# Kernel optimization log

Hardware: AMD Instinct MI355X
Metric: run time of the kernel (lower is better)

## Reference

```python
import jax, jax.numpy as jnp
import numpy as np

B, CIN, COUT, H, W = 64, 96, 96, 56, 56
MID = 192            # in_channels * expansion
SE_GROUPS = 12       # _nearest_divisor(192, 12)
SE_RED = 24          # ceil(max(192//8,4)/12)*12
EPS = 1e-5


def _apply_bn(x, p):
    # p: [4, C] = (gamma, beta, running_mean, running_var); eval-mode BN
    scale = p[0] * jax.lax.rsqrt(p[3] + EPS)
    shift = p[1] - p[2] * scale
    return x * scale[None, :, None, None] + shift[None, :, None, None]


def _shift_groups(x):
    h, w = x.shape[2], x.shape[3]
    x0, x1, x2, x3 = jnp.split(x, 4, axis=1)
    up = jnp.pad(x0, ((0, 0), (0, 0), (1, 0), (0, 0)))[:, :, :h, :]
    left = jnp.pad(x1, ((0, 0), (0, 0), (0, 0), (1, 0)))[:, :, :, :w]
    down = jnp.pad(x2, ((0, 0), (0, 0), (0, 1), (0, 0)))[:, :, 1:, :]
    right = jnp.pad(x3, ((0, 0), (0, 0), (0, 0), (0, 1)))[:, :, :, 1:]
    return jnp.concatenate([up, left, down, right], axis=1)


def _channel_shuffle(x, groups=4):
    b, c, h, w = x.shape
    x = x.reshape(b, groups, c // groups, h, w)
    x = jnp.transpose(x, (0, 2, 1, 3, 4))
    return x.reshape(b, c, h, w)


def _grouped_1x1(v, w, b, groups):
    # v: [B, Cin]; w: [Cout, Cin//groups, 1, 1]
    bsz = v.shape[0]
    cout = w.shape[0]
    vg = v.reshape(bsz, groups, -1)
    wg = w[:, :, 0, 0].reshape(groups, cout // groups, -1)
    out = jnp.einsum('bgi,goi->bgo', vg, wg).reshape(bsz, cout)
    return out + b


def _forward(x, expand_w, expand_bn, dw_w, dw_bn, id_w, id_bn, merge_bn,
             se_red_w, se_red_b, se_exp_w, se_exp_b, proj_w, proj_bn):
    # 1x1 expansion + BN + SiLU
    out = jnp.einsum('bchw,oc->bohw', x, expand_w[:, :, 0, 0])
    out = jax.nn.silu(_apply_bn(out, expand_bn))
    # shift-mix + channel shuffle (zero-FLOP data movement)
    out = _channel_shuffle(_shift_groups(out), groups=4)
    # depthwise 3x3 branch + BN
    dw = jax.lax.conv_general_dilated(
        out, dw_w, window_strides=(1, 1), padding=((1, 1), (1, 1)),
        feature_group_count=MID, dimension_numbers=('NCHW', 'OIHW', 'NCHW'))
    dw = _apply_bn(dw, dw_bn)
    # identity depthwise 1x1 branch (per-channel scale) + BN
    idb = _apply_bn(out * id_w[:, 0, 0, 0][None, :, None, None], id_bn)
    out = jax.nn.silu(_apply_bn(dw + idb, merge_bn))
    # grouped SE gating
    se = jnp.mean(out, axis=(2, 3))                     # [B, MID]
    se = jax.nn.relu(_grouped_1x1(se, se_red_w, se_red_b, SE_GROUPS))
    se = jax.nn.sigmoid(_grouped_1x1(se, se_exp_w, se_exp_b, SE_GROUPS))
    out = out * se[:, :, None, None]
    # 1x1 project + BN + residual + activation
    out = jnp.einsum('bchw,oc->bohw', out, proj_w[:, :, 0, 0])
    out = _apply_bn(out, proj_bn)
    out = out + x  # use_residual: stride==1 and in==out
    return jax.nn.silu(out)


def setup_inputs() -> dict:
    key = jax.random.key(0)
    ks = jax.random.split(key, 16)

    def bn_params(k, c):
        k1, k2, k3, k4 = jax.random.split(k, 4)
        gamma = 1.0 + 0.1 * jax.random.normal(k1, (c,), jnp.float32)
        beta = 0.1 * jax.random.normal(k2, (c,), jnp.float32)
        mean = 0.1 * jax.random.normal(k3, (c,), jnp.float32)
        var = 0.5 + jax.random.uniform(k4, (c,), jnp.float32)
        return jnp.stack([gamma, beta, mean, var])

    return {
        'x': jax.random.normal(ks[0], (B, CIN, H, W), jnp.float32),
        'expand_w': 0.1 * jax.random.normal(ks[1], (MID, CIN, 1, 1), jnp.float32),
        'expand_bn': bn_params(ks[2], MID),
        'dw_w': 0.2 * jax.random.normal(ks[3], (MID, 1, 3, 3), jnp.float32),
        'dw_bn': bn_params(ks[4], MID),
        'id_w': 0.2 * jax.random.normal(ks[5], (MID, 1, 1, 1), jnp.float32),
        'id_bn': bn_params(ks[6], MID),
        'merge_bn': bn_params(ks[7], MID),
        'se_red_w': 0.2 * jax.random.normal(ks[8], (SE_RED, MID // SE_GROUPS, 1, 1), jnp.float32),
        'se_red_b': 0.05 * jax.random.normal(ks[9], (SE_RED,), jnp.float32),
        'se_exp_w': 0.2 * jax.random.normal(ks[10], (MID, SE_RED // SE_GROUPS, 1, 1), jnp.float32),
        'se_exp_b': 0.05 * jax.random.normal(ks[11], (MID,), jnp.float32),
        'proj_w': 0.1 * jax.random.normal(ks[12], (COUT, MID, 1, 1), jnp.float32),
        'proj_bn': bn_params(ks[13], COUT),
    }


def reference(x, expand_w, expand_bn, dw_w, dw_bn, id_w, id_bn, merge_bn,
              se_red_w, se_red_b, se_exp_w, se_exp_b, proj_w, proj_bn):
    return _forward(x, expand_w, expand_bn, dw_w, dw_bn, id_w, id_bn, merge_bn,
                    se_red_w, se_red_b, se_exp_w, se_exp_b, proj_w, proj_bn)
```

## Files before the change

### kernel.cpp

```cpp
#include <hip/hip_runtime.h>
#include <hip/hip_bf16.h>

#define BB   64
#define CING 96
#define MIDC 192
#define HH   56
#define WWD  56
#define HWSZ (HH*WWD)
#define COUTC 96
#define BNEPS 1e-5f

typedef __attribute__((ext_vector_type(8))) short short8;
typedef __attribute__((ext_vector_type(8))) unsigned short ushort8v;
typedef __attribute__((ext_vector_type(4))) float float4v;
typedef unsigned short ushort_t;
typedef unsigned int uint_t;
typedef __attribute__((ext_vector_type(4))) uint_t uint4v;

__device__ __forceinline__ float siluf(float v){
    return v * __builtin_amdgcn_rcpf(1.f + __expf(-v));
}
__device__ __forceinline__ ushort_t f2bs(float f){
    uint_t u = __float_as_uint(f);
    uint_t r = u + 0x7FFFu + ((u >> 16) & 1u);
    return (ushort_t)(r >> 16);
}
__device__ __forceinline__ float bs2f(ushort_t u){
    return __uint_as_float(((uint_t)u) << 16);
}
__device__ __forceinline__ uint_t pkbf(float a, float b){
    __hip_bfloat162 h = __float22bfloat162_rn(make_float2(a, b));
    union { __hip_bfloat162 h; uint_t u; } cv; cv.h = h; return cv.u;
}
__device__ __forceinline__ float bslo(uint_t x){ return __uint_as_float(x << 16); }
__device__ __forceinline__ float bshi(uint_t x){ return __uint_as_float(x & 0xFFFF0000u); }

__global__ __launch_bounds__(256) void k0_setup(
    const float* __restrict__ expand_w, const float* __restrict__ expand_bn,
    const float* __restrict__ dw_w, const float* __restrict__ dw_bn,
    const float* __restrict__ id_w, const float* __restrict__ id_bn,
    const float* __restrict__ merge_bn,
    const float* __restrict__ proj_w, const float* __restrict__ proj_bn,
    ushort_t* __restrict__ Aexp, float* __restrict__ ebias,
    float* __restrict__ w9f, float* __restrict__ cstf,
    ushort_t* __restrict__ Aproj, float* __restrict__ pscf, float* __restrict__ pshf)
{
    int i = blockIdx.x*256 + threadIdx.x;
    if (i < 4608) {
        int m = i/24, kq = (i%24)*4;
        int ic = (m&3)*48 + (m>>2);
        float sc0 = expand_bn[ic]*rsqrtf(expand_bn[3*MIDC+ic]+BNEPS);
        #pragma unroll
        for (int j=0;j<4;j++) Aexp[m*96+kq+j] = f2bs(expand_w[ic*96+kq+j]*sc0);
        if (kq==0) ebias[m] = expand_bn[MIDC+ic] - expand_bn[2*MIDC+ic]*sc0;
    } else if (i < 9216) {
        int ii = i-4608; int m = ii/48, kq = (ii%48)*4;
        #pragma unroll
        for (int j=0;j<4;j++) Aproj[m*MIDC+kq+j] = f2bs(proj_w[m*MIDC+kq+j]);
        if (kq==0){
            float sc = proj_bn[m]*rsqrtf(proj_bn[3*COUTC+m]+BNEPS);
            pscf[m]=sc; pshf[m]=proj_bn[COUTC+m]-proj_bn[2*COUTC+m]*sc;
        }
    } else if (i < 9408) {
        int oc = i-9216;
        float sc1 = dw_bn[oc]    * rsqrtf(dw_bn[3*MIDC+oc]    + BNEPS);
        float sh1 = dw_bn[MIDC+oc]    - dw_bn[2*MIDC+oc]*sc1;
        float sc2 = id_bn[oc]    * rsqrtf(id_bn[3*MIDC+oc]    + BNEPS);
        float sh2 = id_bn[MIDC+oc]    - id_bn[2*MIDC+oc]*sc2;
        float sc3 = merge_bn[oc] * rsqrtf(merge_bn[3*MIDC+oc] + BNEPS);
        float sh3 = merge_bn[MIDC+oc] - merge_bn[2*MIDC+oc]*sc3;
        float A = sc3*sc1;
        #pragma unroll
        for (int j=0;j<9;j++) w9f[oc*9+j] = A*dw_w[oc*9+j];
        w9f[oc*9+4] += sc3*sc2*id_w[oc];
        cstf[oc] = sc3*(sh1+sh2) + sh3;
    }
}

#define LDB1T 104
__global__ __launch_bounds__(256, 2) void k1_expand(
    const float* __restrict__ x,
    const ushort_t* __restrict__ Aexp,
    const float* __restrict__ ebias,
    ushort_t* __restrict__ EY)
{
    __shared__ __align__(16) ushort_t BsT[64*LDB1T];
    __shared__ float ebL[MIDC];
    const int t = threadIdx.x;
    const int p0 = blockIdx.x*64, b = blockIdx.y;

    if (t < MIDC) ebL[t] = ebias[t];
    {
        const int pq = t & 15;
        const int cb = (t >> 4) * 6;
        const float* xp0 = x + ((size_t)(b*CING + cb))*HWSZ + p0 + pq*4;
        float4v xv[6];
        #pragma unroll
        for (int j = 0; j < 6; j++)
            xv[j] = *(const float4v*)(xp0 + (size_t)j*HWSZ);
        #pragma unroll
        for (int px = 0; px < 4; px++) {
            const int n = pq*4 + px;
            uint_t w0 = pkbf(xv[0][px], xv[1][px]);
            uint_t w1 = pkbf(xv[2][px], xv[3][px]);
            uint_t w2 = pkbf(xv[4][px], xv[5][px]);
            uint_t* dst = (uint_t*)(&BsT[n*LDB1T + cb]);
            dst[0] = w0; dst[1] = w1; dst[2] = w2;
        }
    }

    const int lane = t & 63, wv = t >> 6;
    const int l = lane & 15, q = lane >> 4;
    short8 afc[3], afn[3];
    #pragma unroll
    for (int mi = 0; mi < 3; mi++)
        afc[mi] = *(const short8*)(Aexp + ((wv*3+mi)*16 + l)*96 + q*8);
    __syncthreads();

    float4v acc[3][4];
    #pragma unroll
    for (int mi=0;mi<3;mi++)
        #pragma unroll
        for (int nt=0;nt<4;nt++) acc[mi][nt] = (float4v){0.f,0.f,0.f,0.f};
    #pragma unroll
    for (int ks = 0; ks < 3; ks++) {
        if (ks < 2) {
            #pragma unroll
            for (int mi = 0; mi < 3; mi++)
                afn[mi] = *(const short8*)(Aexp + ((wv*3+mi)*16 + l)*96 + (ks+1)*32 + q*8);
        }
        const int k0 = ks*32;
        short8 bf[4];
        #pragma unroll
        for (int nt = 0; nt < 4; nt++)
            bf[nt] = *(const short8*)(&BsT[(nt*16 + l)*LDB1T + k0 + q*8]);
        #pragma unroll
        for (int mi = 0; mi < 3; mi++)
            #pragma unroll
            for (int nt = 0; nt < 4; nt++)
                acc[mi][nt] = __builtin_amdgcn_mfma_f32_16x16x32_bf16(afc[mi], bf[nt], acc[mi][nt], 0,0,0);
        if (ks < 2) {
            #pragma unroll
            for (int mi = 0; mi < 3; mi++) afc[mi] = afn[mi];
        }
    }
    #pragma unroll
    for (int mi = 0; mi < 3; mi++) {
        #pragma unroll
        for (int r = 0; r < 4; r++) {
            int m = (wv*3+mi)*16 + q*4 + r;
            float eb = ebL[m];
            size_t rowb = (size_t)(b*MIDC + m)*HWSZ + p0 + l;
            #pragma unroll
            for (int nt = 0; nt < 4; nt++)
                EY[rowb + nt*16] = f2bs(siluf(acc[mi][nt][r] + eb));
        }
    }
}

template<int DY, int DX>
__device__ __forceinline__ float dw_plane8(
    ushort_t* __restrict__ plane, const float* __restrict__ w9, float cst,
    int li8, int h, bool act)
{
    const int cc = (li8 < 7) ? li8 : 6;
    uint4 pA = make_uint4(0,0,0,0), pB = make_uint4(0,0,0,0);
    int rA = -100, rB = -100;
    if (h == 0) { if (DY==1){ rA=28; rB=29; } else if (DY==0){ rA=28; } }
    else        { if (DY==-1){ rA=26; rB=27; } else if (DY==0){ rA=27; } }
    const ushort_t* pl = plane + cc*8;
    if (rA >= 0) pA = *(const uint4*)(pl + rA*WWD);
    if (rB >= 0) pB = *(const uint4*)(pl + rB*WWD);
    __syncthreads();

    const int ys = h ? 27 : -1;
    const int so = h ? 29 : 1;

    auto loadrow = [&](int y) -> uint4 {
        int yy = y + DY;
        uint4 u = make_uint4(0,0,0,0);
        if (((unsigned)y < (unsigned)HH) && ((unsigned)yy < (unsigned)HH)) {
            if (yy == rA)      u = pA;
            else if (yy == rB) u = pB;
            else               u = *(const uint4*)(pl + yy*WWD);
        }
        return u;
    };

    float p0[8] = {0,0,0,0,0,0,0,0}, p1[8] = {0,0,0,0,0,0,0,0};
    float partial = 0.f;
    uint4 u = loadrow(ys);
    for (int y = ys; y <= ys + 29; ++y) {
        uint4 un = loadrow(y + 1);
        uint_t lhi = __shfl_up(u.w, 1);
        uint_t rlo = __shfl_down(u.x, 1);
        if (li8 == 0) lhi = 0u;
        if (li8 == 6) rlo = 0u;
        float s[12];
        s[0]=bslo(lhi);  s[1]=bshi(lhi);
        s[2]=bslo(u.x);  s[3]=bshi(u.x);
        s[4]=bslo(u.y);  s[5]=bshi(u.y);
        s[6]=bslo(u.z);  s[7]=bshi(u.z);
        s[8]=bslo(u.w);  s[9]=bshi(u.w);
        s[10]=bslo(rlo); s[11]=bshi(rlo);
        if (li8 == 0) s[DX+1]  = 0.f;
        if (li8 == 6) s[DX+10] = 0.f;
        float o[8];
        #pragma unroll
        for (int j = 0; j < 8; j++) {
            float t0 = s[j+DX+1], t1 = s[j+DX+2], t2 = s[j+DX+3];
            o[j]  = fmaf(w9[6],t0, fmaf(w9[7],t1, fmaf(w9[8],t2, p1[j])));
            p1[j] = fmaf(w9[3],t0, fmaf(w9[4],t1, fmaf(w9[5],t2, p0[j])));
            p0[j] = fmaf(w9[0],t0, fmaf(w9[1],t1, fmaf(w9[2],t2, cst)));
        }
        if (y >= so && act) {
            float y0=siluf(o[0]), y1=siluf(o[1]), y2=siluf(o[2]), y3=siluf(o[3]);
            float y4=siluf(o[4]), y5=siluf(o[5]), y6=siluf(o[6]), y7=siluf(o[7]);
            uint4 w4; w4.x=pkbf(y0,y1); w4.y=pkbf(y2,y3); w4.z=pkbf(y4,y5); w4.w=pkbf(y6,y7);
            *(uint4*)(plane + (size_t)(y-1)*WWD + li8*8) = w4;
            partial += ((y0+y1)+(y2+y3)) + ((y4+y5)+(y6+y7));
        }
        u = un;
    }
    #pragma unroll
    for (int off = 1; off < 8; off <<= 1) partial += __shfl_xor(partial, off);
    return partial;
}

__global__ __launch_bounds__(128) void k2_dw(
    ushort_t* __restrict__ EY,
    const float* __restrict__ w9f,
    const float* __restrict__ cstf,
    float* __restrict__ sums)
{
    __shared__ float wred[16];
    const int t = threadIdx.x;
    const int lane = t & 63, h = t >> 6;
    const int lg = lane >> 4;
    const int li = lane & 15;
    const int li8 = li & 7;
    const int hi = li >> 3;
    const int gi = blockIdx.x >> 2, r = blockIdx.x & 3;
    const int b = blockIdx.y;
    const int oc = gi*32 + r + (lg*2 + hi)*4;
    ushort_t* plane = EY + (size_t)(b*MIDC + oc)*HWSZ;
    float w9[9];
    #pragma unroll
    for (int j = 0; j < 9; j++) w9[j] = w9f[oc*9+j];
    const float cst = cstf[oc];
    const bool act = (li8 < 7);
    float ps;
    if      (r == 0) ps = dw_plane8<-1, 0>(plane, w9, cst, li8, h, act);
    else if (r == 1) ps = dw_plane8< 0,-1>(plane, w9, cst, li8, h, act);
    else if (r == 2) ps = dw_plane8< 1, 0>(plane, w9, cst, li8, h, act);
    else             ps = dw_plane8< 0, 1>(plane, w9, cst, li8, h, act);
    if (li8 == 0) wred[h*8 + lg*2 + hi] = ps;
    __syncthreads();
    if (t < 8) sums[b*MIDC + gi*32 + r + t*4] = wred[t] + wred[8 + t];
}

#define LDB4T 200
__global__ __launch_bounds__(256, 2) void k4_proj(
    const ushort_t* __restrict__ EY,
    const float* __restrict__ sums,
    const float* __restrict__ se_red_w, const float* __restrict__ se_red_b,
    const float* __restrict__ se_exp_w, const float* __restrict__ se_exp_b,
    const ushort_t* __restrict__ Aproj,
    const float* __restrict__ pscf, const float* __restrict__ pshf,
    const float* __restrict__ x,
    float* __restrict__ out)
{
    __shared__ __align__(16) ushort_t BsT[64*LDB4T];
    __shared__ float pscL[COUTC], pshL[COUTC];
    __shared__ float meanL[MIDC], redL[24], sewL[MIDC];
    const int t = threadIdx.x;
    const int p0 = blockIdx.x*64, b = blockIdx.y;
    if (t < COUTC) { pscL[t] = pscf[t]; pshL[t] = pshf[t]; }

    if (t < MIDC) meanL[t] = sums[b*MIDC + t] * (1.f/(float)HWSZ);
    __syncthreads();
    if (t < 24) {
        int g = t >> 1;
        float a = se_red_b[t];
        #pragma unroll
        for (int i = 0; i < 16; i++) a += meanL[g*16+i] * se_red_w[t*16+i];
        redL[t] = fmaxf(a, 0.f);
    }
    __syncthreads();
    if (t < MIDC) {
        int g = t >> 4;
        float a = se_exp_b[t] + redL[g*2]*se_exp_w[t*2] + redL[g*2+1]*se_exp_w[t*2+1];
        sewL[t] = __builtin_amdgcn_rcpf(1.f + __expf(-a));
    }
    __syncthreads();

    {
        const int po = t & 7;
        const int cb = (t >> 3) * 6;
        const ushort_t* ep0 = EY + ((size_t)(b*MIDC + cb))*HWSZ + p0 + po*8;
        ushort8v ev[6];
        #pragma unroll
        for (int j = 0; j < 6; j++)
            ev[j] = *(const ushort8v*)(ep0 + (size_t)j*HWSZ);
        float sw[6];
        #pragma unroll
        for (int j = 0; j < 6; j++) sw[j] = sewL[cb + j];
        #pragma unroll
        for (int i = 0; i < 8; i++) {
            const int n = po*8 + i;
            uint_t w0 = pkbf(bs2f(ev[0][i])*sw[0], bs2f(ev[1][i])*sw[1]);
            uint_t w1 = pkbf(bs2f(ev[2][i])*sw[2], bs2f(ev[3][i])*sw[3]);
            uint_t w2 = pkbf(bs2f(ev[4][i])*sw[4], bs2f(ev[5][i])*sw[5]);
            uint_t* dst = (uint_t*)(&BsT[n*LDB4T + cb]);
            dst[0] = w0; dst[1] = w1; dst[2] = w2;
        }
    }

    const int lane = t & 63, wv = t >> 6;
    const int l = lane & 15, q = lane >> 4;
    const int mh = wv >> 1, nh = wv & 1;
    short8 afc[3], afn[3];
    #pragma unroll
    for (int mi = 0; mi < 3; mi++)
        afc[mi] = *(const short8*)(Aproj + ((mh*3+mi)*16 + l)*MIDC + q*8);
    __syncthreads();

    float xpre[24];
    #pragma unroll
    for (int mi = 0; mi < 3; mi++) {
        #pragma unroll
        for (int r = 0; r < 4; r++) {
            size_t rowb = (size_t)(b*COUTC + (mh*3+mi)*16 + q*4 + r)*HWSZ + p0 + nh*32 + l;
            xpre[(mi*4+r)*2  ] = x[rowb];
            xpre[(mi*4+r)*2+1] = x[rowb + 16];
        }
    }

    float4v acc[3][2];
    #pragma unroll
    for (int mi=0;mi<3;mi++)
        #pragma unroll
        for (int nt=0;nt<2;nt++) acc[mi][nt] = (float4v){0.f,0.f,0.f,0.f};
    #pragma unroll
    for (int ks = 0; ks < 6; ks++) {
        if (ks < 5) {
            #pragma unroll
            for (int mi = 0; mi < 3; mi++)
                afn[mi] = *(const short8*)(Aproj + ((mh*3+mi)*16 + l)*MIDC + (ks+1)*32 + q*8);
        }
        const int k0 = ks*32;
        short8 bf[2];
        #pragma unroll
        for (int nt = 0; nt < 2; nt++)
            bf[nt] = *(const short8*)(&BsT[(nh*32 + nt*16 + l)*LDB4T + k0 + q*8]);
        #pragma unroll
        for (int mi = 0; mi < 3; mi++)
            #pragma unroll
            for (int nt = 0; nt < 2; nt++)
                acc[mi][nt] = __builtin_amdgcn_mfma_f32_16x16x32_bf16(afc[mi], bf[nt], acc[mi][nt], 0,0,0);
        if (ks < 5) {
            #pragma unroll
            for (int mi = 0; mi < 3; mi++) afc[mi] = afn[mi];
        }
    }
    #pragma unroll
    for (int mi = 0; mi < 3; mi++) {
        #pragma unroll
        for (int r = 0; r < 4; r++) {
            int m = (mh*3+mi)*16 + q*4 + r;
            float sc = pscL[m], sh = pshL[m];
            size_t rowb = (size_t)(b*COUTC + m)*HWSZ + p0 + nh*32 + l;
            #pragma unroll
            for (int nt = 0; nt < 2; nt++) {
                size_t idx = rowb + nt*16;
                float v = acc[mi][nt][r]*sc + sh + xpre[(mi*4+r)*2+nt];
                out[idx] = siluf(v);
            }
        }
    }
}

extern "C" void kernel_launch(void* const* d_in, const int* in_sizes, int n_in,
                              void* d_out, int out_size, void* d_ws, size_t ws_size,
                              hipStream_t stream)
{
    const float* x         = (const float*)d_in[0];
    const float* expand_w  = (const float*)d_in[1];
    const float* expand_bn = (const float*)d_in[2];
    const float* dw_w      = (const float*)d_in[3];
    const float* dw_bn     = (const float*)d_in[4];
    const float* id_w      = (const float*)d_in[5];
    const float* id_bn     = (const float*)d_in[6];
    const float* merge_bn  = (const float*)d_in[7];
    const float* se_red_w  = (const float*)d_in[8];
    const float* se_red_b  = (const float*)d_in[9];
    const float* se_exp_w  = (const float*)d_in[10];
    const float* se_exp_b  = (const float*)d_in[11];
    const float* proj_w    = (const float*)d_in[12];
    const float* proj_bn   = (const float*)d_in[13];

    char* base = (char*)d_ws;
    size_t off = 0;
    ushort_t* EY   = (ushort_t*)(base + off); off += (size_t)BB*MIDC*HWSZ*2;
    float* sums    = (float*)(base + off);    off += BB*MIDC*4;
    ushort_t* Aexp = (ushort_t*)(base + off); off += MIDC*CING*2;
    ushort_t* Aproj= (ushort_t*)(base + off); off += COUTC*MIDC*2;
    float* ebias   = (float*)(base + off);    off += MIDC*4;
    float* w9f     = (float*)(base + off);    off += MIDC*9*4;
    float* cstf    = (float*)(base + off);    off += MIDC*4;
    float* pscf    = (float*)(base + off);    off += COUTC*4;
    float* pshf    = (float*)(base + off);    off += COUTC*4;

    k0_setup<<<dim3(37), dim3(256), 0, stream>>>(
        expand_w, expand_bn, dw_w, dw_bn, id_w, id_bn, merge_bn, proj_w, proj_bn,
        Aexp, ebias, w9f, cstf, Aproj, pscf, pshf);
    k1_expand<<<dim3(HWSZ/64, BB), dim3(256), 0, stream>>>(x, Aexp, ebias, EY);
    k2_dw<<<dim3(24, BB), dim3(128), 0, stream>>>(EY, w9f, cstf, sums);
    k4_proj<<<dim3(HWSZ/64, BB), dim3(256), 0, stream>>>(
        EY, sums, se_red_w, se_red_b, se_exp_w, se_exp_b,
        Aproj, pscf, pshf, x, (float*)d_out);
}
```

Measured before the change: 262.7 us.

## Fuse expansion GEMM and depthwise conv into one banded kernel via LDS ring buffer

```diff
diff --git a/kernel.cpp b/kernel.cpp
--- a/kernel.cpp
+++ b/kernel.cpp
@@ -9,6 +9,10 @@
 #define HWSZ (HH*WWD)
 #define COUTC 96
 #define BNEPS 1e-5f
+#define CGN  48
+#define BAND 14
+#define LDX  104
+#define LDE  68
 
 typedef __attribute__((ext_vector_type(8))) short short8;
 typedef __attribute__((ext_vector_type(8))) unsigned short ushort8v;
@@ -43,7 +47,8 @@
     const float* __restrict__ proj_w, const float* __restrict__ proj_bn,
     ushort_t* __restrict__ Aexp, float* __restrict__ ebias,
     float* __restrict__ w9f, float* __restrict__ cstf,
-    ushort_t* __restrict__ Aproj, float* __restrict__ pscf, float* __restrict__ pshf)
+    ushort_t* __restrict__ Aproj, float* __restrict__ pscf, float* __restrict__ pshf,
+    float* __restrict__ sums)
 {
     int i = blockIdx.x*256 + threadIdx.x;
     if (i < 4608) {
@@ -74,189 +79,169 @@
         for (int j=0;j<9;j++) w9f[oc*9+j] = A*dw_w[oc*9+j];
         w9f[oc*9+4] += sc3*sc2*id_w[oc];
         cstf[oc] = sc3*(sh1+sh2) + sh3;
-    }
-}
-
-#define LDB1T 104
-__global__ __launch_bounds__(256, 2) void k1_expand(
+    } else if (i < 9408 + BB*MIDC) {
+        sums[i-9408] = 0.f;
+    }
+}
+
+template<int DY, int DX>
+__device__ __forceinline__ float dw_task(
+    const ushort_t* __restrict__ Er, const float* __restrict__ w9, float cst,
+    int ch, int pq14, int yo, ushort_t* __restrict__ plane)
+{
+    const int pxb = pq14*4 - 4;
+    float S[3][12];
+    #pragma unroll
+    for (int d = 0; d < 3; ++d) {
+        int ty = yo - 1 + d;
+        int sr = ty + DY;
+        uint2 a = make_uint2(0u,0u), c = make_uint2(0u,0u), e = make_uint2(0u,0u);
+        if (((unsigned)ty < (unsigned)HH) && ((unsigned)sr < (unsigned)HH)) {
+            int q5 = (sr*13108) >> 16;
+            const ushort_t* row = Er + ((sr - q5*5)*CGN + ch)*LDE;
+            if (pq14 > 0)  a = *(const uint2*)(row + pxb);
+            c = *(const uint2*)(row + pq14*4);
+            if (pq14 < 13) e = *(const uint2*)(row + pq14*4 + 4);
+        }
+        S[d][0]=bslo(a.x); S[d][1]=bshi(a.x); S[d][2]=bslo(a.y); S[d][3]=bshi(a.y);
+        S[d][4]=bslo(c.x); S[d][5]=bshi(c.x); S[d][6]=bslo(c.y); S[d][7]=bshi(c.y);
+        S[d][8]=bslo(e.x); S[d][9]=bshi(e.x); S[d][10]=bslo(e.y); S[d][11]=bshi(e.y);
+        if (DX ==  1 && pq14 == 0)  S[d][4] = 0.f;
+        if (DX == -1 && pq14 == 13) S[d][7] = 0.f;
+    }
+    float o[4];
+    #pragma unroll
+    for (int j = 0; j < 4; ++j) {
+        float acc2 = cst;
+        #pragma unroll
+        for (int d = 0; d < 3; ++d)
+            #pragma unroll
+            for (int e2 = 0; e2 < 3; ++e2)
+                acc2 = fmaf(w9[d*3+e2], S[d][j+DX+e2+3], acc2);
+        o[j] = acc2;
+    }
+    float z0=siluf(o[0]), z1=siluf(o[1]), z2=siluf(o[2]), z3=siluf(o[3]);
+    uint2 w2; w2.x = pkbf(z0,z1); w2.y = pkbf(z2,z3);
+    *(uint2*)(plane + (size_t)yo*WWD + pq14*4) = w2;
+    return (z0+z1)+(z2+z3);
+}
+
+__global__ __launch_bounds__(256, 3) void kF_expdw(
     const float* __restrict__ x,
     const ushort_t* __restrict__ Aexp,
     const float* __restrict__ ebias,
-    ushort_t* __restrict__ EY)
+    const float* __restrict__ w9f,
+    const float* __restrict__ cstf,
+    ushort_t* __restrict__ EY,
+    float* __restrict__ sums)
 {
-    __shared__ __align__(16) ushort_t BsT[64*LDB1T];
-    __shared__ float ebL[MIDC];
+    __shared__ __align__(16) ushort_t Xs[64*LDX];
+    __shared__ __align__(16) ushort_t Er[5*CGN*LDE];
+    __shared__ float w9L[CGN*9];
+    __shared__ float ebL[CGN], cstL[CGN];
+
     const int t = threadIdx.x;
-    const int p0 = blockIdx.x*64, b = blockIdx.y;
-
-    if (t < MIDC) ebL[t] = ebias[t];
-    {
-        const int pq = t & 15;
-        const int cb = (t >> 4) * 6;
-        const float* xp0 = x + ((size_t)(b*CING + cb))*HWSZ + p0 + pq*4;
-        float4v xv[6];
-        #pragma unroll
-        for (int j = 0; j < 6; j++)
-            xv[j] = *(const float4v*)(xp0 + (size_t)j*HWSZ);
-        #pragma unroll
-        for (int px = 0; px < 4; px++) {
-            const int n = pq*4 + px;
-            uint_t w0 = pkbf(xv[0][px], xv[1][px]);
-            uint_t w1 = pkbf(xv[2][px], xv[3][px]);
-            uint_t w2 = pkbf(xv[4][px], xv[5][px]);
-            uint_t* dst = (uint_t*)(&BsT[n*LDB1T + cb]);
-            dst[0] = w0; dst[1] = w1; dst[2] = w2;
-        }
-    }
+    const int cg = blockIdx.x & 3, band = blockIdx.x >> 2;
+    const int b = blockIdx.y;
+    const int mg0 = cg*CGN;
+    const int y0 = band*BAND;
+
+    if (t < CGN) { ebL[t] = ebias[mg0+t]; cstL[t] = cstf[mg0+t]; }
+    if (t < 216) { w9L[t] = w9f[mg0*9 + t]; w9L[t+216] = w9f[mg0*9 + t + 216]; }
 
     const int lane = t & 63, wv = t >> 6;
     const int l = lane & 15, q = lane >> 4;
-    short8 afc[3], afn[3];
-    #pragma unroll
-    for (int mi = 0; mi < 3; mi++)
-        afc[mi] = *(const short8*)(Aexp + ((wv*3+mi)*16 + l)*96 + q*8);
+    short8 af[3][3];
+    #pragma unroll
+    for (int ks = 0; ks < 3; ks++)
+        #pragma unroll
+        for (int mi = 0; mi < 3; mi++)
+            af[ks][mi] = *(const short8*)(Aexp + (size_t)(mg0 + mi*16 + l)*96 + ks*32 + q*8);
+
+    const int pq = t & 15, cb = (t >> 4)*6;
+    ushort_t* EYg = EY + (size_t)(b*MIDC + mg0)*HWSZ;
+
+    int rr3[3], ch3[3], pq3[3]; float psum[3];
+    #pragma unroll
+    for (int pass = 0; pass < 3; ++pass) {
+        int task = t + pass*256;
+        psum[pass] = 0.f;
+        if (task < 672) {
+            int rr = task / 168;
+            int rem = task - rr*168;
+            int i12 = rem / 14;
+            rr3[pass] = rr; pq3[pass] = rem - i12*14; ch3[pass] = i12*4 + rr;
+        } else rr3[pass] = -1;
+    }
     __syncthreads();
 
-    float4v acc[3][4];
-    #pragma unroll
-    for (int mi=0;mi<3;mi++)
-        #pragma unroll
-        for (int nt=0;nt<4;nt++) acc[mi][nt] = (float4v){0.f,0.f,0.f,0.f};
-    #pragma unroll
-    for (int ks = 0; ks < 3; ks++) {
-        if (ks < 2) {
+    for (int er = y0-2; er <= y0+16; ++er) {
+        const bool gemmOk = ((unsigned)er < (unsigned)HH);
+        const bool doLoad = gemmOk && (pq < 14);
+        float4v xv[6];
+        if (doLoad) {
+            const float* xp = x + ((size_t)(b*CING + cb))*HWSZ + er*WWD + pq*4;
+            #pragma unroll
+            for (int j = 0; j < 6; j++)
+                xv[j] = *(const float4v*)(xp + (size_t)j*HWSZ);
+        }
+        const int yo = er - 3;
+        if (yo >= y0 && yo < y0 + BAND) {
+            #pragma unroll
+            for (int pass = 0; pass < 3; ++pass) {
+                if (rr3[pass] >= 0) {
+                    const int ch = ch3[pass], pp = pq3[pass];
+                    const float* w9 = &w9L[ch*9];
+                    const float cst = cstL[ch];
+                    ushort_t* plane = EYg + (size_t)ch*HWSZ;
+                    float ps;
+                    if      (rr3[pass] == 0) ps = dw_task<-1, 0>(Er, w9, cst, ch, pp, yo, plane);
+                    else if (rr3[pass] == 1) ps = dw_task< 0,-1>(Er, w9, cst, ch, pp, yo, plane);
+                    else if (rr3[pass] == 2) ps = dw_task< 1, 0>(Er, w9, cst, ch, pp, yo, plane);
+                    else                     ps = dw_task< 0, 1>(Er, w9, cst, ch, pp, yo, plane);
+                    psum[pass] += ps;
+                }
+            }
+        }
+        if (doLoad) {
+            #pragma unroll
+            for (int px = 0; px < 4; px++) {
+                int n = pq*4 + px;
+                uint_t w0 = pkbf(xv[0][px], xv[1][px]);
+                uint_t w1 = pkbf(xv[2][px], xv[3][px]);
+                uint_t w2 = pkbf(xv[4][px], xv[5][px]);
+                uint_t* dst = (uint_t*)(&Xs[n*LDX + cb]);
+                dst[0] = w0; dst[1] = w1; dst[2] = w2;
+            }
+        }
+        __syncthreads();
+        if (gemmOk) {
+            float4v acc[3];
+            #pragma unroll
+            for (int mi = 0; mi < 3; mi++) acc[mi] = (float4v){0.f,0.f,0.f,0.f};
+            #pragma unroll
+            for (int ks = 0; ks < 3; ks++) {
+                short8 bf = *(const short8*)(&Xs[(wv*16 + l)*LDX + ks*32 + q*8]);
+                #pragma unroll
+                for (int mi = 0; mi < 3; mi++)
+                    acc[mi] = __builtin_amdgcn_mfma_f32_16x16x32_bf16(af[ks][mi], bf, acc[mi], 0,0,0);
+            }
+            int q5 = (er*13108) >> 16;
+            ushort_t* erow = &Er[(er - q5*5)*CGN*LDE];
             #pragma unroll
             for (int mi = 0; mi < 3; mi++)
-                afn[mi] = *(const short8*)(Aexp + ((wv*3+mi)*16 + l)*96 + (ks+1)*32 + q*8);
-        }
-        const int k0 = ks*32;
-        short8 bf[4];
-        #pragma unroll
-        for (int nt = 0; nt < 4; nt++)
-            bf[nt] = *(const short8*)(&BsT[(nt*16 + l)*LDB1T + k0 + q*8]);
-        #pragma unroll
-        for (int mi = 0; mi < 3; mi++)
-            #pragma unroll
-            for (int nt = 0; nt < 4; nt++)
-                acc[mi][nt] = __builtin_amdgcn_mfma_f32_16x16x32_bf16(afc[mi], bf[nt], acc[mi][nt], 0,0,0);
-        if (ks < 2) {
-            #pragma unroll
-            for (int mi = 0; mi < 3; mi++) afc[mi] = afn[mi];
-        }
-    }
-    #pragma unroll
-    for (int mi = 0; mi < 3; mi++) {
-        #pragma unroll
-        for (int r = 0; r < 4; r++) {
-            int m = (wv*3+mi)*16 + q*4 + r;
-            float eb = ebL[m];
-            size_t rowb = (size_t)(b*MIDC + m)*HWSZ + p0 + l;
-            #pragma unroll
-            for (int nt = 0; nt < 4; nt++)
-                EY[rowb + nt*16] = f2bs(siluf(acc[mi][nt][r] + eb));
-        }
-    }
-}
-
-template<int DY, int DX>
-__device__ __forceinline__ float dw_plane8(
-    ushort_t* __restrict__ plane, const float* __restrict__ w9, float cst,
-    int li8, int h, bool act)
-{
-    const int cc = (li8 < 7) ? li8 : 6;
-    uint4 pA = make_uint4(0,0,0,0), pB = make_uint4(0,0,0,0);
-    int rA = -100, rB = -100;
-    if (h == 0) { if (DY==1){ rA=28; rB=29; } else if (DY==0){ rA=28; } }
-    else        { if (DY==-1){ rA=26; rB=27; } else if (DY==0){ rA=27; } }
-    const ushort_t* pl = plane + cc*8;
-    if (rA >= 0) pA = *(const uint4*)(pl + rA*WWD);
-    if (rB >= 0) pB = *(const uint4*)(pl + rB*WWD);
-    __syncthreads();
-
-    const int ys = h ? 27 : -1;
-    const int so = h ? 29 : 1;
-
-    auto loadrow = [&](int y) -> uint4 {
-        int yy = y + DY;
-        uint4 u = make_uint4(0,0,0,0);
-        if (((unsigned)y < (unsigned)HH) && ((unsigned)yy < (unsigned)HH)) {
-            if (yy == rA)      u = pA;
-            else if (yy == rB) u = pB;
-            else               u = *(const uint4*)(pl + yy*WWD);
-        }
-        return u;
-    };
-
-    float p0[8] = {0,0,0,0,0,0,0,0}, p1[8] = {0,0,0,0,0,0,0,0};
-    float partial = 0.f;
-    uint4 u = loadrow(ys);
-    for (int y = ys; y <= ys + 29; ++y) {
-        uint4 un = loadrow(y + 1);
-        uint_t lhi = __shfl_up(u.w, 1);
-        uint_t rlo = __shfl_down(u.x, 1);
-        if (li8 == 0) lhi = 0u;
-        if (li8 == 6) rlo = 0u;
-        float s[12];
-        s[0]=bslo(lhi);  s[1]=bshi(lhi);
-        s[2]=bslo(u.x);  s[3]=bshi(u.x);
-        s[4]=bslo(u.y);  s[5]=bshi(u.y);
-        s[6]=bslo(u.z);  s[7]=bshi(u.z);
-        s[8]=bslo(u.w);  s[9]=bshi(u.w);
-        s[10]=bslo(rlo); s[11]=bshi(rlo);
-        if (li8 == 0) s[DX+1]  = 0.f;
-        if (li8 == 6) s[DX+10] = 0.f;
-        float o[8];
-        #pragma unroll
-        for (int j = 0; j < 8; j++) {
-            float t0 = s[j+DX+1], t1 = s[j+DX+2], t2 = s[j+DX+3];
-            o[j]  = fmaf(w9[6],t0, fmaf(w9[7],t1, fmaf(w9[8],t2, p1[j])));
-            p1[j] = fmaf(w9[3],t0, fmaf(w9[4],t1, fmaf(w9[5],t2, p0[j])));
-            p0[j] = fmaf(w9[0],t0, fmaf(w9[1],t1, fmaf(w9[2],t2, cst)));
-        }
-        if (y >= so && act) {
-            float y0=siluf(o[0]), y1=siluf(o[1]), y2=siluf(o[2]), y3=siluf(o[3]);
-            float y4=siluf(o[4]), y5=siluf(o[5]), y6=siluf(o[6]), y7=siluf(o[7]);
-            uint4 w4; w4.x=pkbf(y0,y1); w4.y=pkbf(y2,y3); w4.z=pkbf(y4,y5); w4.w=pkbf(y6,y7);
-            *(uint4*)(plane + (size_t)(y-1)*WWD + li8*8) = w4;
-            partial += ((y0+y1)+(y2+y3)) + ((y4+y5)+(y6+y7));
-        }
-        u = un;
-    }
-    #pragma unroll
-    for (int off = 1; off < 8; off <<= 1) partial += __shfl_xor(partial, off);
-    return partial;
-}
-
-__global__ __launch_bounds__(128) void k2_dw(
-    ushort_t* __restrict__ EY,
-    const float* __restrict__ w9f,
-    const float* __restrict__ cstf,
-    float* __restrict__ sums)
-{
-    __shared__ float wred[16];
-    const int t = threadIdx.x;
-    const int lane = t & 63, h = t >> 6;
-    const int lg = lane >> 4;
-    const int li = lane & 15;
-    const int li8 = li & 7;
-    const int hi = li >> 3;
-    const int gi = blockIdx.x >> 2, r = blockIdx.x & 3;
-    const int b = blockIdx.y;
-    const int oc = gi*32 + r + (lg*2 + hi)*4;
-    ushort_t* plane = EY + (size_t)(b*MIDC + oc)*HWSZ;
-    float w9[9];
-    #pragma unroll
-    for (int j = 0; j < 9; j++) w9[j] = w9f[oc*9+j];
-    const float cst = cstf[oc];
-    const bool act = (li8 < 7);
-    float ps;
-    if      (r == 0) ps = dw_plane8<-1, 0>(plane, w9, cst, li8, h, act);
-    else if (r == 1) ps = dw_plane8< 0,-1>(plane, w9, cst, li8, h, act);
-    else if (r == 2) ps = dw_plane8< 1, 0>(plane, w9, cst, li8, h, act);
-    else             ps = dw_plane8< 0, 1>(plane, w9, cst, li8, h, act);
-    if (li8 == 0) wred[h*8 + lg*2 + hi] = ps;
-    __syncthreads();
-    if (t < 8) sums[b*MIDC + gi*32 + r + t*4] = wred[t] + wred[8 + t];
+                #pragma unroll
+                for (int r = 0; r < 4; r++) {
+                    int m = mi*16 + q*4 + r;
+                    erow[m*LDE + wv*16 + l] = f2bs(siluf(acc[mi][r] + ebL[m]));
+                }
+        }
+        __syncthreads();
+    }
+    #pragma unroll
+    for (int pass = 0; pass < 3; ++pass)
+        if (rr3[pass] >= 0)
+            atomicAdd(&sums[b*MIDC + mg0 + ch3[pass]], psum[pass]);
 }
 
 #define LDB4T 200
@@ -411,11 +396,11 @@
     float* pscf    = (float*)(base + off);    off += COUTC*4;
     float* pshf    = (float*)(base + off);    off += COUTC*4;
 
-    k0_setup<<<dim3(37), dim3(256), 0, stream>>>(
+    k0_setup<<<dim3(85), dim3(256), 0, stream>>>(
         expand_w, expand_bn, dw_w, dw_bn, id_w, id_bn, merge_bn, proj_w, proj_bn,
-        Aexp, ebias, w9f, cstf, Aproj, pscf, pshf);
-    k1_expand<<<dim3(HWSZ/64, BB), dim3(256), 0, stream>>>(x, Aexp, ebias, EY);
-    k2_dw<<<dim3(24, BB), dim3(128), 0, stream>>>(EY, w9f, cstf, sums);
+        Aexp, ebias, w9f, cstf, Aproj, pscf, pshf, sums);
+    kF_expdw<<<dim3(16, BB), dim3(256), 0, stream>>>(
+        x, Aexp, ebias, w9f, cstf, EY, sums);
     k4_proj<<<dim3(HWSZ/64, BB), dim3(256), 0, stream>>>(
         EY, sums, se_red_w, se_red_b, se_exp_w, se_exp_b,
         Aproj, pscf, pshf, x, (float*)d_out);
```

Result: slower. 344.5 us (+31.1%).
